# Optimization experiments

Measured on AMD Instinct MI355X. Metric: run time of the kernel, lower is better.

The kernel has to match this reference:

```python
import jax, jax.numpy as jnp
import numpy as np

LMAX, RB, RA, N, D = 4, 12, 11, 131072, 64
S = (LMAX + 1) ** 2


def _assoc_legendre_norm(lmax, x):
    # Fully-normalized associated Legendre P_l^m(x), orthonormal over the sphere
    # (includes sqrt((2l+1)/(4pi) * (l-m)!/(l+m)!)). x: [B] = cos(beta).
    B = x.shape[0]
    s = np.sqrt(np.clip(1.0 - x * x, 0.0, 1.0))
    P = np.zeros((lmax + 1, lmax + 1, B))
    P[0, 0] = np.sqrt(1.0 / (4.0 * np.pi))
    for m in range(1, lmax + 1):
        P[m, m] = -np.sqrt((2.0 * m + 1.0) / (2.0 * m)) * s * P[m - 1, m - 1]
    for m in range(0, lmax):
        P[m + 1, m] = np.sqrt(2.0 * m + 3.0) * x * P[m, m]
    for m in range(0, lmax + 1):
        for l in range(m + 2, lmax + 1):
            a = np.sqrt((4.0 * l * l - 1.0) / (l * l - m * m))
            b = np.sqrt((((l - 1) ** 2 - m * m)) / (4.0 * (l - 1) ** 2 - 1.0))
            P[l, m] = a * (x * P[l - 1, m] - b * P[l - 2, m])
    return P


def _sh_grid(lmax, res_beta, res_alpha):
    # Real orthonormal spherical harmonics sampled on a Gauss-Legendre x uniform-alpha grid,
    # plus quadrature weights so that sum_{b,a} Y_i Y_j qw_b = delta_ij (band-limited).
    x, w = np.polynomial.legendre.leggauss(res_beta)  # nodes in cos(beta)
    alpha = 2.0 * np.pi * np.arange(res_alpha) / res_alpha
    P = _assoc_legendre_norm(lmax, x)  # [L+1, L+1, RB]
    Ssz = (lmax + 1) ** 2
    Y = np.zeros((res_beta, res_alpha, Ssz))
    i = 0
    for l in range(lmax + 1):
        for m in range(-l, l + 1):
            if m < 0:
                ang = np.sqrt(2.0) * np.sin(-m * alpha)
            elif m == 0:
                ang = np.ones_like(alpha)
            else:
                ang = np.sqrt(2.0) * np.cos(m * alpha)
            Y[:, :, i] = P[l, abs(m)][:, None] * ang[None, :]
            i += 1
    qw = w * (2.0 * np.pi / res_alpha)  # beta quadrature * alpha trapezoid weight
    return Y.astype(np.float32), qw.astype(np.float32)


def setup_inputs() -> dict:
    key = jax.random.key(0)
    k1, k2, k3, k4 = jax.random.split(key, 4)
    Y_np, qw_np = _sh_grid(LMAX, RB, RA)
    Y = jnp.asarray(Y_np)                       # [RB, RA, S]
    Yw = Y * jnp.asarray(qw_np)[:, None, None]  # [RB, RA, S] (quadrature-weighted)
    input1 = jax.random.normal(k1, (N, D), dtype=jnp.float32)
    input2 = jax.random.normal(k2, (N, D), dtype=jnp.float32)
    W1 = jax.random.normal(k3, (D, S), dtype=jnp.float32) * 0.1
    W2 = jax.random.normal(k4, (D, S), dtype=jnp.float32) * 0.1
    return {"input1": input1, "input2": input2, "W1": W1, "W2": W2, "Y": Y, "Yw": Yw}


def reference(input1, input2, W1, W2, Y, Yw):
    # linear_in: project input irreps to S2 spherical-harmonic coefficients
    c1 = input1 @ W1  # [N, S]
    c2 = input2 @ W2  # [N, S]
    # ToS2Grid: evaluate band-limited signal on the (beta, alpha) grid
    g1 = jnp.einsum("ns,bas->nba", c1, Y)  # [N, RB, RA]
    g2 = jnp.einsum("ns,bas->nba", c2, Y)
    # pointwise product on the sphere, then FromS2Grid (quadrature projection)
    return jnp.einsum("nba,bas->ns", g1 * g2, Yw)  # [N, S]
```

## Files before the change

### kernel.cpp

```cpp
#include <hip/hip_runtime.h>


typedef _Float16 f16x8 __attribute__((ext_vector_type(8)));
typedef _Float16 f16x4 __attribute__((ext_vector_type(4)));
typedef float f32x4 __attribute__((ext_vector_type(4)));
typedef float f32x4u __attribute__((ext_vector_type(4), aligned(4)));

namespace {
constexpr int kD = 64, kS = 25, kP = 132;
constexpr int kBlock = 256, kM = 256;
constexpr int kYfOff  = 0;
constexpr int kYwOff  = 4608;
constexpr int kScrOff = 9216;
constexpr int kScrRow = 48;
constexpr int kLdsHalfs = 15360;
}

__device__ __forceinline__ f16x8 ld8(const _Float16* p) {
    return *reinterpret_cast<const f16x8*>(p);
}
__device__ __forceinline__ f16x4 ld4(const _Float16* p) {
    return *reinterpret_cast<const f16x4*>(p);
}
__device__ __forceinline__ f16x8 cvt8h(f32x4 u, f32x4 v) {
    f16x8 r;
    r[0] = (_Float16)u[0]; r[1] = (_Float16)u[1];
    r[2] = (_Float16)u[2]; r[3] = (_Float16)u[3];
    r[4] = (_Float16)v[0]; r[5] = (_Float16)v[1];
    r[6] = (_Float16)v[2]; r[7] = (_Float16)v[3];
    return r;
}

__global__ __launch_bounds__(kBlock, 2) void gaunt_fused8(
    const float* __restrict__ in1, const float* __restrict__ in2,
    const float* __restrict__ W1, const float* __restrict__ W2,
    const float* __restrict__ Y,  const float* __restrict__ Yw,
    float* __restrict__ out)
{
    __shared__ _Float16 lds[kLdsHalfs];
    const int tid  = threadIdx.x;
    const int lane = tid & 63;
    const int w    = __builtin_amdgcn_readfirstlane(tid >> 6);
    const int lo16 = lane & 15, quad = lane >> 4;

    for (int pair = tid; pair < 576; pair += kBlock) {
        const int pt = pair >> 6;
        const int ln = pair & 63;
        const int p  = pt * 16 + (ln & 15);
        const int s0 = ((ln >> 4) & 3) * 8;
        f16x8 v;
        #pragma unroll
        for (int j = 0; j < 8; ++j) v[j] = (_Float16)0.f;
        if (p < kP) {
            const float* yp = Y + p * kS + s0;
            if (s0 < 24) {
                const f32x4u u = *reinterpret_cast<const f32x4u*>(yp);
                const f32x4u q = *reinterpret_cast<const f32x4u*>(yp + 4);
                #pragma unroll
                for (int j = 0; j < 4; ++j) {
                    v[j]     = (_Float16)u[j];
                    v[4 + j] = (_Float16)q[j];
                }
            } else {
                v[0] = (_Float16)yp[0];
            }
        }
        *reinterpret_cast<f16x8*>(&lds[kYfOff + (pt * 64 + ln) * 8]) = v;
    }

    for (int e = tid; e < 4608; e += kBlock) {
        const int i = e & 3, ln = (e >> 2) & 63, r = e >> 8;
        const int pt = r % 9, st = r / 9;
        const int p = pt * 16 + ((ln >> 4) & 3) * 4 + i;
        const int s = st * 16 + (ln & 15);
        lds[kYwOff + e] = (s < kS && p < kP) ? (_Float16)Yw[p * kS + s]
                                             : (_Float16)0.f;
    }

    f16x8 w1f[2][2], w2f[2][2];
    #pragma unroll
    for (int st = 0; st < 2; ++st) {
        const int s = st * 16 + lo16;
        #pragma unroll
        for (int ks = 0; ks < 2; ++ks) {
            f16x8 a, b;
            #pragma unroll
            for (int j = 0; j < 8; ++j) { a[j] = (_Float16)0.f; b[j] = (_Float16)0.f; }
            if (s < kS) {
                const int d0 = ks * 32 + quad * 8;
                #pragma unroll
                for (int j = 0; j < 8; ++j) {
                    a[j] = (_Float16)W1[(d0 + j) * kS + s];
                    b[j] = (_Float16)W2[(d0 + j) * kS + s];
                }
            }
            w1f[st][ks] = a; w2f[st][ks] = b;
        }
    }

    __syncthreads();

    const long long base = (long long)blockIdx.x * (kM * kD);
    f16x8 b1[4][2], b2[4][2];
    #pragma unroll
    for (int rt = 0; rt < 4; ++rt) {
        const int row = (4 * w + rt) * 16 + lo16;
        const float* p1 = in1 + base + row * kD + quad * 8;
        const float* p2 = in2 + base + row * kD + quad * 8;
        #pragma unroll
        for (int ks = 0; ks < 2; ++ks) {
            const f32x4 u1 = *reinterpret_cast<const f32x4*>(p1 + ks * 32);
            const f32x4 v1 = *reinterpret_cast<const f32x4*>(p1 + ks * 32 + 4);
            const f32x4 u2 = *reinterpret_cast<const f32x4*>(p2 + ks * 32);
            const f32x4 v2 = *reinterpret_cast<const f32x4*>(p2 + ks * 32 + 4);
            b1[rt][ks] = cvt8h(u1, v1);
            b2[rt][ks] = cvt8h(u2, v2);
        }
    }

    f16x8 c1t[4], c2t[4];
    _Float16* scr = &lds[kScrOff + w * (2 * 16 * kScrRow)];
    #pragma unroll
    for (int rt = 0; rt < 4; ++rt) {
        f32x4 c1[2], c2[2];
        #pragma unroll
        for (int st = 0; st < 2; ++st) {
            c1[st] = (f32x4){0.f, 0.f, 0.f, 0.f};
            c2[st] = (f32x4){0.f, 0.f, 0.f, 0.f};
        }
        #pragma unroll
        for (int st = 0; st < 2; ++st)
            #pragma unroll
            for (int ks = 0; ks < 2; ++ks) {
                c1[st] = __builtin_amdgcn_mfma_f32_16x16x32_f16(b1[rt][ks], w1f[st][ks], c1[st], 0, 0, 0);
                c2[st] = __builtin_amdgcn_mfma_f32_16x16x32_f16(b2[rt][ks], w2f[st][ks], c2[st], 0, 0, 0);
            }
        #pragma unroll
        for (int st = 0; st < 2; ++st)
            #pragma unroll
            for (int i = 0; i < 4; ++i) {
                scr[(quad * 4 + i) * kScrRow + st * 16 + lo16]       = (_Float16)c1[st][i];
                scr[768 + (quad * 4 + i) * kScrRow + st * 16 + lo16] = (_Float16)c2[st][i];
            }
        c1t[rt] = ld8(&scr[lo16 * kScrRow + quad * 8]);
        c2t[rt] = ld8(&scr[768 + lo16 * kScrRow + quad * 8]);
    }

    f32x4 oacc[4][2];
    #pragma unroll
    for (int rt = 0; rt < 4; ++rt)
        #pragma unroll
        for (int st = 0; st < 2; ++st)
            oacc[rt][st] = (f32x4){0.f, 0.f, 0.f, 0.f};

    f16x8 yc  = ld8(&lds[kYfOff + lane * 8]);
    f16x4 yw0 = ld4(&lds[kYwOff + lane * 4]);
    f16x4 yw1 = ld4(&lds[kYwOff + 9 * 256 + lane * 4]);

    #pragma unroll 1
    for (int pt = 0; pt < 9; ++pt) {
        f16x8 yn; f16x4 yw0n, yw1n;
        if (pt < 8) {
            yn   = ld8(&lds[kYfOff + (pt + 1) * 512 + lane * 8]);
            yw0n = ld4(&lds[kYwOff + (pt + 1) * 256 + lane * 4]);
            yw1n = ld4(&lds[kYwOff + (9 + pt + 1) * 256 + lane * 4]);
        }
        #pragma unroll
        for (int rt = 0; rt < 4; ++rt) {
            f32x4 z = (f32x4){0.f, 0.f, 0.f, 0.f};
            f32x4 g1 = __builtin_amdgcn_mfma_f32_16x16x32_f16(yc, c1t[rt], z, 0, 0, 0);
            f32x4 g2 = __builtin_amdgcn_mfma_f32_16x16x32_f16(yc, c2t[rt], z, 0, 0, 0);
            f16x4 h;
            h[0] = (_Float16)(g1[0] * g2[0]);
            h[1] = (_Float16)(g1[1] * g2[1]);
            h[2] = (_Float16)(g1[2] * g2[2]);
            h[3] = (_Float16)(g1[3] * g2[3]);
            oacc[rt][0] = __builtin_amdgcn_mfma_f32_16x16x16f16(yw0, h, oacc[rt][0], 0, 0, 0);
            oacc[rt][1] = __builtin_amdgcn_mfma_f32_16x16x16f16(yw1, h, oacc[rt][1], 0, 0, 0);
        }
        yc = yn; yw0 = yw0n; yw1 = yw1n;
    }

    const long long ob = (long long)blockIdx.x * (kM * kS);
    #pragma unroll
    for (int rt = 0; rt < 4; ++rt) {
        const int row = (4 * w + rt) * 16 + lo16;
        float* rp = out + ob + (long long)row * kS;
        *reinterpret_cast<f32x4u*>(rp + quad * 4) = oacc[rt][0];
        if (quad < 2) {
            *reinterpret_cast<f32x4u*>(rp + 16 + quad * 4) = oacc[rt][1];
        } else if (quad == 2) {
            rp[24] = oacc[rt][1][0];
        }
    }
}

extern "C" void kernel_launch(void* const* d_in, const int* in_sizes, int n_in,
                              void* d_out, int out_size, void* d_ws, size_t ws_size,
                              hipStream_t stream) {
    const float* in1 = (const float*)d_in[0];
    const float* in2 = (const float*)d_in[1];
    const float* W1  = (const float*)d_in[2];
    const float* W2  = (const float*)d_in[3];
    const float* Y   = (const float*)d_in[4];
    const float* Yw  = (const float*)d_in[5];
    float* out = (float*)d_out;
    (void)d_ws; (void)ws_size;

    const int n_rows = in_sizes[0] / kD;
    const int grid = n_rows / kM;
    gaunt_fused8<<<grid, kBlock, 0, stream>>>(in1, in2, W1, W2, Y, Yw, out);
}
```

Measured before the change: 114.5 us.

## Keep projected coefficients in registers and hoist input loads before LDS setup

The first-stage MFMA now computes the transposed product (W as A operand), so each lane's coefficient output is already in the operand layout the grid-evaluation MFMA needs. This removes the per-warp LDS scratch round-trip and its shared-memory footprint, and splits the grid MFMA into two 16x16x16 steps. The global input loads are also issued before the Y/Yw LDS staging so their latency overlaps the table setup. The cost is more live registers, since the input loads are held through setup, and twice as many smaller MFMAs in the inner loop.

```diff
diff --git a/kernel.cpp b/kernel.cpp
--- a/kernel.cpp
+++ b/kernel.cpp
@@ -9,16 +9,11 @@
 namespace {
 constexpr int kD = 64, kS = 25, kP = 132;
 constexpr int kBlock = 256, kM = 256;
-constexpr int kYfOff  = 0;
-constexpr int kYwOff  = 4608;
-constexpr int kScrOff = 9216;
-constexpr int kScrRow = 48;
-constexpr int kLdsHalfs = 15360;
+constexpr int kYfOff = 0;
+constexpr int kYwOff = 4608;
+constexpr int kLdsHalfs = 9216;
 }
 
-__device__ __forceinline__ f16x8 ld8(const _Float16* p) {
-    return *reinterpret_cast<const f16x8*>(p);
-}
 __device__ __forceinline__ f16x4 ld4(const _Float16* p) {
     return *reinterpret_cast<const f16x4*>(p);
 }
@@ -31,7 +26,7 @@
     return r;
 }
 
-__global__ __launch_bounds__(kBlock, 2) void gaunt_fused8(
+__global__ __launch_bounds__(kBlock, 2) void gaunt_fused9(
     const float* __restrict__ in1, const float* __restrict__ in2,
     const float* __restrict__ W1, const float* __restrict__ W2,
     const float* __restrict__ Y,  const float* __restrict__ Yw,
@@ -43,31 +38,30 @@
     const int w    = __builtin_amdgcn_readfirstlane(tid >> 6);
     const int lo16 = lane & 15, quad = lane >> 4;
 
-    for (int pair = tid; pair < 576; pair += kBlock) {
-        const int pt = pair >> 6;
-        const int ln = pair & 63;
-        const int p  = pt * 16 + (ln & 15);
-        const int s0 = ((ln >> 4) & 3) * 8;
-        f16x8 v;
+    const long long base = (long long)blockIdx.x * (kM * kD);
+    f32x4 u1[4][2], v1[4][2], u2[4][2], v2[4][2];
+    #pragma unroll
+    for (int rt = 0; rt < 4; ++rt) {
+        const int row = (4 * w + rt) * 16 + lo16;
+        const float* p1 = in1 + base + row * kD + quad * 8;
+        const float* p2 = in2 + base + row * kD + quad * 8;
         #pragma unroll
-        for (int j = 0; j < 8; ++j) v[j] = (_Float16)0.f;
-        if (p < kP) {
-            const float* yp = Y + p * kS + s0;
-            if (s0 < 24) {
-                const f32x4u u = *reinterpret_cast<const f32x4u*>(yp);
-                const f32x4u q = *reinterpret_cast<const f32x4u*>(yp + 4);
-                #pragma unroll
-                for (int j = 0; j < 4; ++j) {
-                    v[j]     = (_Float16)u[j];
-                    v[4 + j] = (_Float16)q[j];
-                }
-            } else {
-                v[0] = (_Float16)yp[0];
-            }
+        for (int ks = 0; ks < 2; ++ks) {
+            u1[rt][ks] = *reinterpret_cast<const f32x4*>(p1 + ks * 32);
+            v1[rt][ks] = *reinterpret_cast<const f32x4*>(p1 + ks * 32 + 4);
+            u2[rt][ks] = *reinterpret_cast<const f32x4*>(p2 + ks * 32);
+            v2[rt][ks] = *reinterpret_cast<const f32x4*>(p2 + ks * 32 + 4);
         }
-        *reinterpret_cast<f16x8*>(&lds[kYfOff + (pt * 64 + ln) * 8]) = v;
     }
 
+    for (int e = tid; e < 4608; e += kBlock) {
+        const int i = e & 3, ln = (e >> 2) & 63, r = e >> 8;
+        const int pt = r >> 1, st = r & 1;
+        const int p = pt * 16 + (ln & 15);
+        const int s = st * 16 + ((ln >> 4) & 3) * 4 + i;
+        lds[kYfOff + e] = (s < kS && p < kP) ? (_Float16)Y[p * kS + s]
+                                             : (_Float16)0.f;
+    }
     for (int e = tid; e < 4608; e += kBlock) {
         const int i = e & 3, ln = (e >> 2) & 63, r = e >> 8;
         const int pt = r % 9, st = r / 9;
@@ -100,50 +94,35 @@
 
     __syncthreads();
 
-    const long long base = (long long)blockIdx.x * (kM * kD);
     f16x8 b1[4][2], b2[4][2];
     #pragma unroll
-    for (int rt = 0; rt < 4; ++rt) {
-        const int row = (4 * w + rt) * 16 + lo16;
-        const float* p1 = in1 + base + row * kD + quad * 8;
-        const float* p2 = in2 + base + row * kD + quad * 8;
+    for (int rt = 0; rt < 4; ++rt)
         #pragma unroll
         for (int ks = 0; ks < 2; ++ks) {
-            const f32x4 u1 = *reinterpret_cast<const f32x4*>(p1 + ks * 32);
-            const f32x4 v1 = *reinterpret_cast<const f32x4*>(p1 + ks * 32 + 4);
-            const f32x4 u2 = *reinterpret_cast<const f32x4*>(p2 + ks * 32);
-            const f32x4 v2 = *reinterpret_cast<const f32x4*>(p2 + ks * 32 + 4);
-            b1[rt][ks] = cvt8h(u1, v1);
-            b2[rt][ks] = cvt8h(u2, v2);
+            b1[rt][ks] = cvt8h(u1[rt][ks], v1[rt][ks]);
+            b2[rt][ks] = cvt8h(u2[rt][ks], v2[rt][ks]);
         }
-    }
 
-    f16x8 c1t[4], c2t[4];
-    _Float16* scr = &lds[kScrOff + w * (2 * 16 * kScrRow)];
+    f16x4 h1c[4][2], h2c[4][2];
     #pragma unroll
     for (int rt = 0; rt < 4; ++rt) {
-        f32x4 c1[2], c2[2];
         #pragma unroll
         for (int st = 0; st < 2; ++st) {
-            c1[st] = (f32x4){0.f, 0.f, 0.f, 0.f};
-            c2[st] = (f32x4){0.f, 0.f, 0.f, 0.f};
-        }
-        #pragma unroll
-        for (int st = 0; st < 2; ++st)
+            f32x4 c1 = (f32x4){0.f, 0.f, 0.f, 0.f};
+            f32x4 c2 = (f32x4){0.f, 0.f, 0.f, 0.f};
             #pragma unroll
             for (int ks = 0; ks < 2; ++ks) {
-                c1[st] = __builtin_amdgcn_mfma_f32_16x16x32_f16(b1[rt][ks], w1f[st][ks], c1[st], 0, 0, 0);
-                c2[st] = __builtin_amdgcn_mfma_f32_16x16x32_f16(b2[rt][ks], w2f[st][ks], c2[st], 0, 0, 0);
+                c1 = __builtin_amdgcn_mfma_f32_16x16x32_f16(w1f[st][ks], b1[rt][ks], c1, 0, 0, 0);
+                c2 = __builtin_amdgcn_mfma_f32_16x16x32_f16(w2f[st][ks], b2[rt][ks], c2, 0, 0, 0);
             }
-        #pragma unroll
-        for (int st = 0; st < 2; ++st)
+            f16x4 hc1, hc2;
             #pragma unroll
             for (int i = 0; i < 4; ++i) {
-                scr[(quad * 4 + i) * kScrRow + st * 16 + lo16]       = (_Float16)c1[st][i];
-                scr[768 + (quad * 4 + i) * kScrRow + st * 16 + lo16] = (_Float16)c2[st][i];
+                hc1[i] = (_Float16)c1[i];
+                hc2[i] = (_Float16)c2[i];
             }
-        c1t[rt] = ld8(&scr[lo16 * kScrRow + quad * 8]);
-        c2t[rt] = ld8(&scr[768 + lo16 * kScrRow + quad * 8]);
+            h1c[rt][st] = hc1; h2c[rt][st] = hc2;
+        }
     }
 
     f32x4 oacc[4][2];
@@ -153,32 +132,37 @@
         for (int st = 0; st < 2; ++st)
             oacc[rt][st] = (f32x4){0.f, 0.f, 0.f, 0.f};
 
-    f16x8 yc  = ld8(&lds[kYfOff + lane * 8]);
-    f16x4 yw0 = ld4(&lds[kYwOff + lane * 4]);
-    f16x4 yw1 = ld4(&lds[kYwOff + 9 * 256 + lane * 4]);
+    f16x4 yfc[2], yw0c, yw1c;
+    yfc[0] = ld4(&lds[kYfOff + (0 * 2 + 0) * 256 + lane * 4]);
+    yfc[1] = ld4(&lds[kYfOff + (0 * 2 + 1) * 256 + lane * 4]);
+    yw0c   = ld4(&lds[kYwOff + (0 * 9 + 0) * 256 + lane * 4]);
+    yw1c   = ld4(&lds[kYwOff + (1 * 9 + 0) * 256 + lane * 4]);
 
     #pragma unroll 1
     for (int pt = 0; pt < 9; ++pt) {
-        f16x8 yn; f16x4 yw0n, yw1n;
+        f16x4 yfn[2], yw0n, yw1n;
         if (pt < 8) {
-            yn   = ld8(&lds[kYfOff + (pt + 1) * 512 + lane * 8]);
-            yw0n = ld4(&lds[kYwOff + (pt + 1) * 256 + lane * 4]);
-            yw1n = ld4(&lds[kYwOff + (9 + pt + 1) * 256 + lane * 4]);
+            yfn[0] = ld4(&lds[kYfOff + ((pt + 1) * 2 + 0) * 256 + lane * 4]);
+            yfn[1] = ld4(&lds[kYfOff + ((pt + 1) * 2 + 1) * 256 + lane * 4]);
+            yw0n   = ld4(&lds[kYwOff + (0 * 9 + pt + 1) * 256 + lane * 4]);
+            yw1n   = ld4(&lds[kYwOff + (1 * 9 + pt + 1) * 256 + lane * 4]);
         }
         #pragma unroll
         for (int rt = 0; rt < 4; ++rt) {
-            f32x4 z = (f32x4){0.f, 0.f, 0.f, 0.f};
-            f32x4 g1 = __builtin_amdgcn_mfma_f32_16x16x32_f16(yc, c1t[rt], z, 0, 0, 0);
-            f32x4 g2 = __builtin_amdgcn_mfma_f32_16x16x32_f16(yc, c2t[rt], z, 0, 0, 0);
+            const f32x4 z = (f32x4){0.f, 0.f, 0.f, 0.f};
+            f32x4 g1 = __builtin_amdgcn_mfma_f32_16x16x16f16(yfc[0], h1c[rt][0], z, 0, 0, 0);
+            g1       = __builtin_amdgcn_mfma_f32_16x16x16f16(yfc[1], h1c[rt][1], g1, 0, 0, 0);
+            f32x4 g2 = __builtin_amdgcn_mfma_f32_16x16x16f16(yfc[0], h2c[rt][0], z, 0, 0, 0);
+            g2       = __builtin_amdgcn_mfma_f32_16x16x16f16(yfc[1], h2c[rt][1], g2, 0, 0, 0);
             f16x4 h;
             h[0] = (_Float16)(g1[0] * g2[0]);
             h[1] = (_Float16)(g1[1] * g2[1]);
             h[2] = (_Float16)(g1[2] * g2[2]);
             h[3] = (_Float16)(g1[3] * g2[3]);
-            oacc[rt][0] = __builtin_amdgcn_mfma_f32_16x16x16f16(yw0, h, oacc[rt][0], 0, 0, 0);
-            oacc[rt][1] = __builtin_amdgcn_mfma_f32_16x16x16f16(yw1, h, oacc[rt][1], 0, 0, 0);
+            oacc[rt][0] = __builtin_amdgcn_mfma_f32_16x16x16f16(yw0c, h, oacc[rt][0], 0, 0, 0);
+            oacc[rt][1] = __builtin_amdgcn_mfma_f32_16x16x16f16(yw1c, h, oacc[rt][1], 0, 0, 0);
         }
-        yc = yn; yw0 = yw0n; yw1 = yw1n;
+        yfc[0] = yfn[0]; yfc[1] = yfn[1]; yw0c = yw0n; yw1c = yw1n;
     }
 
     const long long ob = (long long)blockIdx.x * (kM * kS);
@@ -209,5 +193,5 @@
 
     const int n_rows = in_sizes[0] / kD;
     const int grid = n_rows / kM;
-    gaunt_fused8<<<grid, kBlock, 0, stream>>>(in1, in2, W1, W2, Y, Yw, out);
+    gaunt_fused9<<<grid, kBlock, 0, stream>>>(in1, in2, W1, W2, Y, Yw, out);
 }
```

New measurement: 115.8 us. Within noise of the previous version (+1.1%).
